# Kernel tuning notes

Hardware: AMD Instinct MI355X
Metric: run time of the kernel (lower is better)

Reference implementation:

```python
import jax, jax.numpy as jnp
import numpy as np

B, S, D, H = 2, 2048, 1024, 16
HD = D // H
NEG = -9000000000000000.0


def setup_inputs() -> dict:
    key = jax.random.key(0)
    ks = jax.random.split(key, 12)
    scale = 1.0 / np.sqrt(D)
    inp = {
        "k": jax.random.normal(ks[0], (B, S, D), jnp.float32),
        "q": jax.random.normal(ks[1], (B, S, D), jnp.float32),
        "v": jax.random.normal(ks[2], (B, S, D), jnp.float32),
        # causal mask, float (0/1), shape [B, 1, S, S] as expected by __call__
        "mask": jnp.broadcast_to(jnp.tril(jnp.ones((S, S), jnp.float32))[None, None], (B, 1, S, S)),
        "Wq": jax.random.normal(ks[3], (D, D), jnp.float32) * scale,
        "bq": jnp.zeros((D,), jnp.float32),
        "Wk": jax.random.normal(ks[4], (D, D), jnp.float32) * scale,
        "bk": jnp.zeros((D,), jnp.float32),
        "Wv": jax.random.normal(ks[5], (D, D), jnp.float32) * scale,
        "bv": jnp.zeros((D,), jnp.float32),
        "Wo": jax.random.normal(ks[6], (D, D), jnp.float32) * scale,
        "bo": jnp.zeros((D,), jnp.float32),
    }
    return inp


def _split_heads(x):
    # [B, S, D] -> [B, H, S, HD]
    return x.reshape(B, S, H, HD).transpose(0, 2, 1, 3)


def reference(k, q, v, mask, Wq, bq, Wk, bk, Wv, bv, Wo, bo):
    keys = _split_heads(k @ Wk + bk)
    queries = _split_heads(q @ Wq + bq)
    values = _split_heads(v @ Wv + bv)
    # scaled dot product with materialized scores (faithful to source)
    logits = jnp.einsum("bhqd,bhkd->bhqk", queries, keys) / np.sqrt(HD)
    logits = jnp.where(mask == 0, NEG, logits)
    attention = jax.nn.softmax(logits, axis=-1)
    out = jnp.einsum("bhqk,bhkd->bhqd", attention, values)
    out = out.transpose(0, 2, 1, 3).reshape(B, S, D)
    o = out @ Wo + bo
    return (o, attention)
```

## Files before the change

### kernel.cpp

```cpp
#include <hip/hip_runtime.h>
#include <stdint.h>

typedef unsigned short u16;
typedef short short8 __attribute__((ext_vector_type(8)));
typedef unsigned short ushort8 __attribute__((ext_vector_type(8)));
typedef float f32x4 __attribute__((ext_vector_type(4)));

#define S_LEN 2048
#define D_DIM 1024
#define H_NUM 16
#define HD_DIM 64
#define NEGBIG (-1e30f)

__device__ __forceinline__ float bf2f(u16 u) {
  union { uint32_t i; float f; } x; x.i = ((uint32_t)u) << 16; return x.f;
}
__device__ __forceinline__ u16 f2bf(float f) {
  union { float f; uint32_t i; } x; x.f = f;
  uint32_t u = x.i;
  uint32_t r = (u + 0x7fffu + ((u >> 16) & 1u)) >> 16;
  return (u16)r;
}
__device__ __forceinline__ f32x4 mfma16(short8 a, short8 b, f32x4 c) {
  return __builtin_amdgcn_mfma_f32_16x16x32_bf16(a, b, c, 0, 0, 0);
}
__device__ __forceinline__ bool mask_is_f32(const void* mask) {
  return *(const float*)mask == 1.0f;
}

__global__ __launch_bounds__(256) void conv_qkv(const void* __restrict__ q,
                                                const void* __restrict__ k,
                                                const void* __restrict__ v,
                                                u16* __restrict__ out,
                                                const void* __restrict__ mask) {
  bool isf32 = mask_is_f32(mask);
  int z = blockIdx.y;
  const void* src = (z == 0) ? q : (z == 1) ? k : v;
  size_t i = ((size_t)blockIdx.x * 256 + threadIdx.x) * 8;
  u16* dst = out + (size_t)z * 4194304;
  if (isf32) {
    const f32x4* p = (const f32x4*)((const float*)src + i);
    f32x4 a = p[0], b = p[1];
    ushort8 o;
#pragma unroll
    for (int j = 0; j < 4; j++) { o[j] = f2bf(a[j]); o[4 + j] = f2bf(b[j]); }
    *(ushort8*)(dst + i) = o;
  } else {
    *(ushort8*)(dst + i) = *(const ushort8*)((const u16*)src + i);
  }
}

__global__ __launch_bounds__(256) void wtrans(const void* __restrict__ w0,
                                              const void* __restrict__ w1,
                                              const void* __restrict__ w2,
                                              const void* __restrict__ w3,
                                              u16* __restrict__ dstBase,
                                              const void* __restrict__ mask) {
  bool isf32 = mask_is_f32(mask);
  int y = blockIdx.y;
  const void* W = (y == 0) ? w0 : (y == 1) ? w1 : (y == 2) ? w2 : w3;
  u16* out = dstBase + (size_t)y * 1048576;
  __shared__ u16 t[64][65];
  int tile = blockIdx.x;
  int r0 = (tile >> 4) * 64, c0 = (tile & 15) * 64;
  int tid = threadIdx.x;
  int rr = tid >> 6, cc = tid & 63;
#pragma unroll
  for (int i = 0; i < 16; i++) {
    int r = i * 4 + rr;
    size_t idx = (size_t)(r0 + r) * 1024 + c0 + cc;
    t[r][cc] = isf32 ? f2bf(((const float*)W)[idx]) : ((const u16*)W)[idx];
  }
  __syncthreads();
#pragma unroll
  for (int i = 0; i < 16; i++) {
    int r = i * 4 + rr;
    out[(size_t)(c0 + r) * 1024 + r0 + cc] = t[cc][r];
  }
}

__global__ __launch_bounds__(256) void conv_bias(const void* __restrict__ b0,
                                                 const void* __restrict__ b1,
                                                 const void* __restrict__ b2,
                                                 const void* __restrict__ b3,
                                                 float* __restrict__ out,
                                                 const void* __restrict__ mask) {
  bool isf32 = mask_is_f32(mask);
  int y = blockIdx.y;
  const void* b = (y == 0) ? b0 : (y == 1) ? b1 : (y == 2) ? b2 : b3;
  int i = blockIdx.x * 256 + threadIdx.x;
  float v = isf32 ? ((const float*)b)[i] : bf2f(((const u16*)b)[i]);
  out[y * 1024 + i] = v;
}

__global__ __launch_bounds__(256) void v_transpose(const u16* __restrict__ V,
                                                   u16* __restrict__ Vt) {
  __shared__ u16 t[64][65];
  int bh = blockIdx.x, st = blockIdx.y;
  int b = bh >> 4, h = bh & 15;
  int tid = threadIdx.x;
  int rr = tid >> 6, cc = tid & 63;
#pragma unroll
  for (int i = 0; i < 16; i++) {
    int r = i * 4 + rr;
    t[r][cc] = V[(size_t)(b * S_LEN + st * 64 + r) * D_DIM + h * HD_DIM + cc];
  }
  __syncthreads();
#pragma unroll
  for (int i = 0; i < 16; i++) {
    int r = i * 4 + rr;
    Vt[(size_t)(bh * HD_DIM + r) * S_LEN + st * 64 + cc] = t[cc][r];
  }
}

__device__ __forceinline__ void gemm_body(const u16* __restrict__ A,
                                          const u16* __restrict__ Bt,
                                          const float* __restrict__ bias,
                                          void* __restrict__ C, bool cf32,
                                          int M, int N, int K, int m0, int n0) {
  __shared__ __align__(16) u16 lA[2][128 * 32];
  __shared__ __align__(16) u16 lB[2][128 * 32];
  int tid = threadIdx.x;
  int lane = tid & 63, w = tid >> 6;
  int wr = w >> 1, wc = w & 1;
  f32x4 acc[4][4] = {};
  int rs = tid >> 2, c8 = tid & 3;
  ushort8 ra[2], rb[2];
  const int nk = K >> 5;
#pragma unroll
  for (int p = 0; p < 2; p++) {
    ra[p] = *(const ushort8*)(A + (size_t)(m0 + p * 64 + rs) * K + c8 * 8);
    rb[p] = *(const ushort8*)(Bt + (size_t)(n0 + p * 64 + rs) * K + c8 * 8);
  }
#pragma unroll
  for (int p = 0; p < 2; p++) {
    *(ushort8*)(&lA[0][(p * 64 + rs) * 32 + c8 * 8]) = ra[p];
    *(ushort8*)(&lB[0][(p * 64 + rs) * 32 + c8 * 8]) = rb[p];
  }
  int cur = 0;
  for (int kt = 0; kt < nk; kt++) {
    __syncthreads();
    if (kt + 1 < nk) {
#pragma unroll
      for (int p = 0; p < 2; p++) {
        ra[p] = *(const ushort8*)(A + (size_t)(m0 + p * 64 + rs) * K + (kt + 1) * 32 + c8 * 8);
        rb[p] = *(const ushort8*)(Bt + (size_t)(n0 + p * 64 + rs) * K + (kt + 1) * 32 + c8 * 8);
      }
    }
    short8 af[4], bf[4];
#pragma unroll
    for (int i = 0; i < 4; i++) {
      af[i] = *(const short8*)(&lA[cur][(wr * 64 + i * 16 + (lane & 15)) * 32 + (lane >> 4) * 8]);
      bf[i] = *(const short8*)(&lB[cur][(wc * 64 + i * 16 + (lane & 15)) * 32 + (lane >> 4) * 8]);
    }
#pragma unroll
    for (int i = 0; i < 4; i++)
#pragma unroll
      for (int j = 0; j < 4; j++)
        acc[i][j] = mfma16(af[i], bf[j], acc[i][j]);
    if (kt + 1 < nk) {
#pragma unroll
      for (int p = 0; p < 2; p++) {
        *(ushort8*)(&lA[cur ^ 1][(p * 64 + rs) * 32 + c8 * 8]) = ra[p];
        *(ushort8*)(&lB[cur ^ 1][(p * 64 + rs) * 32 + c8 * 8]) = rb[p];
      }
    }
    cur ^= 1;
  }
#pragma unroll
  for (int j = 0; j < 4; j++) {
    float bv = bias[n0 + wc * 64 + j * 16 + (lane & 15)];
#pragma unroll
    for (int i = 0; i < 4; i++) {
#pragma unroll
      for (int jj = 0; jj < 4; jj++) {
        int row = m0 + wr * 64 + i * 16 + ((lane >> 4) << 2) + jj;
        int col = n0 + wc * 64 + j * 16 + (lane & 15);
        float val = acc[i][j][jj] + bv;
        if (cf32) ((float*)C)[(size_t)row * N + col] = val;
        else ((u16*)C)[(size_t)row * N + col] = f2bf(val);
      }
    }
  }
}

__global__ __launch_bounds__(256, 2) void qkv_gemm(const u16* __restrict__ Ab,
                                                   const u16* __restrict__ WTall,
                                                   const float* __restrict__ biasF,
                                                   u16* __restrict__ outbase) {
  int z = blockIdx.z;
  gemm_body(Ab + (size_t)z * 4194304, WTall + (size_t)z * 1048576, biasF + z * 1024,
            outbase + (size_t)z * 4194304, false,
            4096, 1024, 1024, blockIdx.y * 128, blockIdx.x * 128);
}

__global__ __launch_bounds__(256, 2) void gemm_bt(const u16* __restrict__ A,
                                                  const u16* __restrict__ Bt,
                                                  const float* __restrict__ bias,
                                                  void* __restrict__ dout,
                                                  const void* __restrict__ mask) {
  bool isf32 = mask_is_f32(mask);
  gemm_body(A, Bt, bias, dout, isf32,
            4096, 1024, 1024, blockIdx.y * 128, blockIdx.x * 128);
}

__global__ __launch_bounds__(256, 3) void attn_fused(const u16* __restrict__ Qg,
                                                     const u16* __restrict__ Kg,
                                                     const u16* __restrict__ VtG,
                                                     void* __restrict__ dout,
                                                     u16* __restrict__ ctx,
                                                     const void* __restrict__ mask) {
  bool isf32 = mask_is_f32(mask);
  int x = blockIdx.x, bh = blockIdx.y;
  int b = bh >> 4, h = bh & 15;
  int tid = threadIdx.x, lane = tid & 63, w = tid >> 6;
  __shared__ __align__(16) u16 lQ[128 * 72];
  __shared__ __align__(16) u16 lK[64 * 72];
  __shared__ __align__(16) u16 lV[64 * 72];
  __shared__ __align__(16) u16 lP[64 * 72];

#pragma unroll
  for (int s = 0; s < 2; s++) {
    int qt = (s == 0) ? x : 31 - x;
    int q0 = qt * 64;
#pragma unroll
    for (int p = 0; p < 2; p++) {
      int idx = p * 256 + tid;
      int r = idx >> 3, c8i = idx & 7;
      ushort8 v = *(const ushort8*)(Qg + (size_t)(b * S_LEN + q0 + r) * D_DIM + h * HD_DIM + c8i * 8);
      *(ushort8*)(&lQ[(s * 64 + r) * 72 + c8i * 8]) = v;
    }
  }

  for (int s = 0; s < 2; s++) {
    int qt = (s == 0) ? x : 31 - x;
    int q0 = qt * 64;
    int nkv = qt + 1;

    auto stageK = [&](int kt) {
#pragma unroll
      for (int p = 0; p < 2; p++) {
        int idx = p * 256 + tid;
        int r = idx >> 3, c8i = idx & 7;
        ushort8 v = *(const ushort8*)(Kg + (size_t)(b * S_LEN + kt * 64 + r) * D_DIM + h * HD_DIM + c8i * 8);
        *(ushort8*)(&lK[r * 72 + c8i * 8]) = v;
      }
    };
    auto stageV = [&](int kt) {
#pragma unroll
      for (int p = 0; p < 2; p++) {
        int idx = p * 256 + tid;
        int r = idx >> 3, c8i = idx & 7;
        ushort8 v = *(const ushort8*)(VtG + (size_t)(bh * HD_DIM + r) * S_LEN + kt * 64 + c8i * 8);
        *(ushort8*)(&lV[r * 72 + c8i * 8]) = v;
      }
    };
    auto computeS = [&](int kt, f32x4 (&sacc)[4]) {
      short8 af[2], bfr[4][2];
#pragma unroll
      for (int ks = 0; ks < 2; ks++)
        af[ks] = *(const short8*)(&lQ[(s * 64 + w * 16 + (lane & 15)) * 72 + ks * 32 + (lane >> 4) * 8]);
#pragma unroll
      for (int j = 0; j < 4; j++)
#pragma unroll
        for (int ks = 0; ks < 2; ks++)
          bfr[j][ks] = *(const short8*)(&lK[(j * 16 + (lane & 15)) * 72 + ks * 32 + (lane >> 4) * 8]);
#pragma unroll
      for (int j = 0; j < 4; j++) {
        f32x4 a = {0.f, 0.f, 0.f, 0.f};
        a = mfma16(af[0], bfr[j][0], a);
        a = mfma16(af[1], bfr[j][1], a);
        sacc[j] = a;
      }
      bool needmask = (kt == qt);
#pragma unroll
      for (int j = 0; j < 4; j++)
#pragma unroll
        for (int jj = 0; jj < 4; jj++) {
          float sv = sacc[j][jj] * 0.125f;
          if (needmask) {
            int row = q0 + w * 16 + ((lane >> 4) << 2) + jj;
            int col = kt * 64 + j * 16 + (lane & 15);
            if (col > row) sv = NEGBIG;
          }
          sacc[j][jj] = sv;
        }
    };

    float m_[4], l_[4];
#pragma unroll
    for (int jj = 0; jj < 4; jj++) { m_[jj] = NEGBIG; l_[jj] = 0.f; }

    for (int kt = 0; kt < nkv; kt++) {
      __syncthreads();
      stageK(kt);
      __syncthreads();
      f32x4 sacc[4];
      computeS(kt, sacc);
#pragma unroll
      for (int jj = 0; jj < 4; jj++) {
        float vm = fmaxf(fmaxf(sacc[0][jj], sacc[1][jj]),
                         fmaxf(sacc[2][jj], sacc[3][jj]));
        vm = fmaxf(vm, __shfl_xor(vm, 1));
        vm = fmaxf(vm, __shfl_xor(vm, 2));
        vm = fmaxf(vm, __shfl_xor(vm, 4));
        vm = fmaxf(vm, __shfl_xor(vm, 8));
        float nm = fmaxf(m_[jj], vm);
        float ss = __expf(sacc[0][jj] - nm) + __expf(sacc[1][jj] - nm) +
                   __expf(sacc[2][jj] - nm) + __expf(sacc[3][jj] - nm);
        ss += __shfl_xor(ss, 1);
        ss += __shfl_xor(ss, 2);
        ss += __shfl_xor(ss, 4);
        ss += __shfl_xor(ss, 8);
        l_[jj] = l_[jj] * __expf(m_[jj] - nm) + ss;
        m_[jj] = nm;
      }
    }
    float invl[4];
#pragma unroll
    for (int jj = 0; jj < 4; jj++) invl[jj] = 1.f / l_[jj];

    f32x4 oacc[4] = {};

    for (int kt = 0; kt < nkv; kt++) {
      __syncthreads();
      stageK(kt);
      stageV(kt);
      __syncthreads();
      f32x4 sacc[4];
      computeS(kt, sacc);
#pragma unroll
      for (int j = 0; j < 4; j++)
#pragma unroll
        for (int jj = 0; jj < 4; jj++) {
          float p = __expf(sacc[j][jj] - m_[jj]) * invl[jj];
          lP[(w * 16 + ((lane >> 4) << 2) + jj) * 72 + j * 16 + (lane & 15)] = f2bf(p);
        }
      __syncthreads();
      {
        int rbase = tid >> 5, c2 = tid & 31;
        if (isf32) {
          float* attnF = (float*)dout + 4194304;
#pragma unroll
          for (int it = 0; it < 8; it++) {
            int r = it * 8 + rbase;
            float2 vv;
            vv.x = bf2f(lP[r * 72 + c2 * 2]);
            vv.y = bf2f(lP[r * 72 + c2 * 2 + 1]);
            *(float2*)(attnF + ((size_t)bh * S_LEN + q0 + r) * S_LEN + kt * 64 + c2 * 2) = vv;
          }
        } else {
          u16* attnB = (u16*)dout + 4194304;
#pragma unroll
          for (int it = 0; it < 8; it++) {
            int r = it * 8 + rbase;
            uint32_t vv = *(const uint32_t*)(&lP[r * 72 + c2 * 2]);
            *(uint32_t*)(attnB + ((size_t)bh * S_LEN + q0 + r) * S_LEN + kt * 64 + c2 * 2) = vv;
          }
        }
      }
      short8 pa[2], vb[4][2];
#pragma unroll
      for (int ks = 0; ks < 2; ks++)
        pa[ks] = *(const short8*)(&lP[(w * 16 + (lane & 15)) * 72 + ks * 32 + (lane >> 4) * 8]);
#pragma unroll
      for (int f = 0; f < 4; f++)
#pragma unroll
        for (int ks = 0; ks < 2; ks++)
          vb[f][ks] = *(const short8*)(&lV[(f * 16 + (lane & 15)) * 72 + ks * 32 + (lane >> 4) * 8]);
#pragma unroll
      for (int f = 0; f < 4; f++) {
        oacc[f] = mfma16(pa[0], vb[f][0], oacc[f]);
        oacc[f] = mfma16(pa[1], vb[f][1], oacc[f]);
      }
    }

    {
      int z0 = nkv * 64;
      if (isf32) {
        int zc4 = (S_LEN - z0) >> 2;
        if (zc4 > 0) {
          f32x4 zz = {0.f, 0.f, 0.f, 0.f};
          float* attnF = (float*)dout + 4194304;
          for (int r = tid >> 5; r < 64; r += 8)
            for (int c = tid & 31; c < zc4; c += 32)
              *(f32x4*)(attnF + ((size_t)bh * S_LEN + q0 + r) * S_LEN + z0 + c * 4) = zz;
        }
      } else {
        int zc8 = (S_LEN - z0) >> 3;
        if (zc8 > 0) {
          ushort8 zz = {0, 0, 0, 0, 0, 0, 0, 0};
          u16* attnB = (u16*)dout + 4194304;
          for (int r = tid >> 5; r < 64; r += 8)
            for (int c = tid & 31; c < zc8; c += 32)
              *(ushort8*)(attnB + ((size_t)bh * S_LEN + q0 + r) * S_LEN + z0 + c * 8) = zz;
        }
      }
    }

#pragma unroll
    for (int f = 0; f < 4; f++)
#pragma unroll
      for (int jj = 0; jj < 4; jj++) {
        int row = q0 + w * 16 + ((lane >> 4) << 2) + jj;
        int col = h * HD_DIM + f * 16 + (lane & 15);
        ctx[(size_t)(b * S_LEN + row) * D_DIM + col] = f2bf(oacc[f][jj]);
      }
  }
}

extern "C" void kernel_launch(void* const* d_in, const int* in_sizes, int n_in,
                              void* d_out, int out_size, void* d_ws, size_t ws_size,
                              hipStream_t stream) {
  const void* kin = d_in[0];
  const void* qin = d_in[1];
  const void* vin = d_in[2];
  const void* mask = d_in[3];
  const void* Wq = d_in[4];
  const void* bq = d_in[5];
  const void* Wk = d_in[6];
  const void* bk = d_in[7];
  const void* Wv = d_in[8];
  const void* bv = d_in[9];
  const void* Wo = d_in[10];
  const void* bo = d_in[11];

  u16* ws = (u16*)d_ws;
  u16* WT = ws;
  float* biasF = (float*)(ws + 4 * 1048576);
  u16* Cb = ws + 4 * 1048576 + 8192;
  u16* Qp = Cb + 3 * 4194304;
  u16* Kp = Qp + 4194304;
  u16* Vp = Kp + 4194304;
  u16* Vt = Vp + 4194304;
  u16* ctx = Vt + 4194304;

  conv_qkv<<<dim3(2048, 3), 256, 0, stream>>>(qin, kin, vin, Cb, mask);
  wtrans<<<dim3(256, 4), 256, 0, stream>>>(Wq, Wk, Wv, Wo, WT, mask);
  conv_bias<<<dim3(4, 4), 256, 0, stream>>>(bq, bk, bv, bo, biasF, mask);
  qkv_gemm<<<dim3(8, 32, 3), 256, 0, stream>>>(Cb, WT, biasF, Qp);
  v_transpose<<<dim3(32, 32), 256, 0, stream>>>(Vp, Vt);
  attn_fused<<<dim3(16, 32), 256, 0, stream>>>(Qp, Kp, Vt, d_out, ctx, mask);
  gemm_bt<<<dim3(8, 32), 256, 0, stream>>>(ctx, WT + 3 * 1048576, biasF + 3072, d_out, mask);
}
```

Baseline: 294.6 us.

## Double-buffer K/V tiles in attention and use async global-to-LDS loads in GEMM

The GEMM now stages A/B tiles straight into LDS with global_load_lds, prefetching the next k-tile while the MFMAs run, with one barrier per iteration. The attention kernel double-buffers K and V in LDS with register prefetch, keeps Q fragments in registers instead of LDS, and writes the attention probabilities directly from registers rather than through an LDS round-trip. This removes barriers and lets loads overlap with compute. In exchange, the direct attention-matrix stores are scalar and less coalesced, and the attention kernel's occupancy hint drops from 3 to 2 blocks per CU.

```diff
diff --git a/kernel.cpp b/kernel.cpp
--- a/kernel.cpp
+++ b/kernel.cpp
@@ -26,6 +26,11 @@
 }
 __device__ __forceinline__ bool mask_is_f32(const void* mask) {
   return *(const float*)mask == 1.0f;
+}
+__device__ __forceinline__ void async_cp16(const u16* g, u16* l) {
+  __builtin_amdgcn_global_load_lds((const __attribute__((address_space(1))) unsigned int*)g,
+                                   (__attribute__((address_space(3))) unsigned int*)l,
+                                   16, 0, 0);
 }
 
 __global__ __launch_bounds__(256) void conv_qkv(const void* __restrict__ q,
@@ -124,29 +129,24 @@
   int lane = tid & 63, w = tid >> 6;
   int wr = w >> 1, wc = w & 1;
   f32x4 acc[4][4] = {};
-  int rs = tid >> 2, c8 = tid & 3;
-  ushort8 ra[2], rb[2];
   const int nk = K >> 5;
-#pragma unroll
-  for (int p = 0; p < 2; p++) {
-    ra[p] = *(const ushort8*)(A + (size_t)(m0 + p * 64 + rs) * K + c8 * 8);
-    rb[p] = *(const ushort8*)(Bt + (size_t)(n0 + p * 64 + rs) * K + c8 * 8);
-  }
-#pragma unroll
-  for (int p = 0; p < 2; p++) {
-    *(ushort8*)(&lA[0][(p * 64 + rs) * 32 + c8 * 8]) = ra[p];
-    *(ushort8*)(&lB[0][(p * 64 + rs) * 32 + c8 * 8]) = rb[p];
-  }
+  int grow = lane >> 2, gcol = (lane & 3) * 8;
+
+#define GEMM_ISSUE(kt, buf)                                                              \
+  {                                                                                      \
+    _Pragma("unroll") for (int p = 0; p < 2; p++) {                                      \
+      async_cp16(A + (size_t)(m0 + p * 64 + w * 16 + grow) * K + (kt) * 32 + gcol,       \
+                 &lA[buf][p * 2048 + w * 512]);                                          \
+      async_cp16(Bt + (size_t)(n0 + p * 64 + w * 16 + grow) * K + (kt) * 32 + gcol,      \
+                 &lB[buf][p * 2048 + w * 512]);                                          \
+    }                                                                                    \
+  }
+
+  GEMM_ISSUE(0, 0);
+  __syncthreads();
   int cur = 0;
   for (int kt = 0; kt < nk; kt++) {
-    __syncthreads();
-    if (kt + 1 < nk) {
-#pragma unroll
-      for (int p = 0; p < 2; p++) {
-        ra[p] = *(const ushort8*)(A + (size_t)(m0 + p * 64 + rs) * K + (kt + 1) * 32 + c8 * 8);
-        rb[p] = *(const ushort8*)(Bt + (size_t)(n0 + p * 64 + rs) * K + (kt + 1) * 32 + c8 * 8);
-      }
-    }
+    if (kt + 1 < nk) GEMM_ISSUE(kt + 1, cur ^ 1);
     short8 af[4], bf[4];
 #pragma unroll
     for (int i = 0; i < 4; i++) {
@@ -158,15 +158,10 @@
 #pragma unroll
       for (int j = 0; j < 4; j++)
         acc[i][j] = mfma16(af[i], bf[j], acc[i][j]);
-    if (kt + 1 < nk) {
-#pragma unroll
-      for (int p = 0; p < 2; p++) {
-        *(ushort8*)(&lA[cur ^ 1][(p * 64 + rs) * 32 + c8 * 8]) = ra[p];
-        *(ushort8*)(&lB[cur ^ 1][(p * 64 + rs) * 32 + c8 * 8]) = rb[p];
-      }
-    }
+    __syncthreads();
     cur ^= 1;
   }
+#undef GEMM_ISSUE
 #pragma unroll
   for (int j = 0; j < 4; j++) {
     float bv = bias[n0 + wc * 64 + j * 16 + (lane & 15)];
@@ -204,7 +199,7 @@
             4096, 1024, 1024, blockIdx.y * 128, blockIdx.x * 128);
 }
 
-__global__ __launch_bounds__(256, 3) void attn_fused(const u16* __restrict__ Qg,
+__global__ __launch_bounds__(256, 2) void attn_fused(const u16* __restrict__ Qg,
                                                      const u16* __restrict__ Kg,
                                                      const u16* __restrict__ VtG,
                                                      void* __restrict__ dout,
@@ -214,62 +209,60 @@
   int x = blockIdx.x, bh = blockIdx.y;
   int b = bh >> 4, h = bh & 15;
   int tid = threadIdx.x, lane = tid & 63, w = tid >> 6;
-  __shared__ __align__(16) u16 lQ[128 * 72];
-  __shared__ __align__(16) u16 lK[64 * 72];
-  __shared__ __align__(16) u16 lV[64 * 72];
+  __shared__ __align__(16) u16 lK[2][64 * 72];
+  __shared__ __align__(16) u16 lV[2][64 * 72];
   __shared__ __align__(16) u16 lP[64 * 72];
 
-#pragma unroll
-  for (int s = 0; s < 2; s++) {
-    int qt = (s == 0) ? x : 31 - x;
-    int q0 = qt * 64;
-#pragma unroll
-    for (int p = 0; p < 2; p++) {
-      int idx = p * 256 + tid;
-      int r = idx >> 3, c8i = idx & 7;
-      ushort8 v = *(const ushort8*)(Qg + (size_t)(b * S_LEN + q0 + r) * D_DIM + h * HD_DIM + c8i * 8);
-      *(ushort8*)(&lQ[(s * 64 + r) * 72 + c8i * 8]) = v;
-    }
-  }
+  float* attnF = (float*)dout + 4194304;
+  u16* attnB = (u16*)dout + 4194304;
+  int sr = tid >> 3, sc8 = (tid & 7) * 8;
 
   for (int s = 0; s < 2; s++) {
     int qt = (s == 0) ? x : 31 - x;
     int q0 = qt * 64;
     int nkv = qt + 1;
 
-    auto stageK = [&](int kt) {
-#pragma unroll
-      for (int p = 0; p < 2; p++) {
-        int idx = p * 256 + tid;
-        int r = idx >> 3, c8i = idx & 7;
-        ushort8 v = *(const ushort8*)(Kg + (size_t)(b * S_LEN + kt * 64 + r) * D_DIM + h * HD_DIM + c8i * 8);
-        *(ushort8*)(&lK[r * 72 + c8i * 8]) = v;
-      }
+    short8 qf[2];
+#pragma unroll
+    for (int ks = 0; ks < 2; ks++)
+      qf[ks] = *(const short8*)(Qg + (size_t)(b * S_LEN + q0 + w * 16 + (lane & 15)) * D_DIM +
+                                h * HD_DIM + ks * 32 + (lane >> 4) * 8);
+
+    ushort8 kreg[2], vreg[2];
+    auto loadK = [&](int kt) {
+#pragma unroll
+      for (int p = 0; p < 2; p++)
+        kreg[p] = *(const ushort8*)(Kg + (size_t)(b * S_LEN + kt * 64 + p * 32 + sr) * D_DIM +
+                                    h * HD_DIM + sc8);
     };
-    auto stageV = [&](int kt) {
-#pragma unroll
-      for (int p = 0; p < 2; p++) {
-        int idx = p * 256 + tid;
-        int r = idx >> 3, c8i = idx & 7;
-        ushort8 v = *(const ushort8*)(VtG + (size_t)(bh * HD_DIM + r) * S_LEN + kt * 64 + c8i * 8);
-        *(ushort8*)(&lV[r * 72 + c8i * 8]) = v;
-      }
+    auto writeK = [&](int buf) {
+#pragma unroll
+      for (int p = 0; p < 2; p++)
+        *(ushort8*)(&lK[buf][(p * 32 + sr) * 72 + sc8]) = kreg[p];
     };
-    auto computeS = [&](int kt, f32x4 (&sacc)[4]) {
-      short8 af[2], bfr[4][2];
-#pragma unroll
-      for (int ks = 0; ks < 2; ks++)
-        af[ks] = *(const short8*)(&lQ[(s * 64 + w * 16 + (lane & 15)) * 72 + ks * 32 + (lane >> 4) * 8]);
+    auto loadV = [&](int kt) {
+#pragma unroll
+      for (int p = 0; p < 2; p++)
+        vreg[p] = *(const ushort8*)(VtG + (size_t)(bh * HD_DIM + p * 32 + sr) * S_LEN +
+                                    kt * 64 + sc8);
+    };
+    auto writeV = [&](int buf) {
+#pragma unroll
+      for (int p = 0; p < 2; p++)
+        *(ushort8*)(&lV[buf][(p * 32 + sr) * 72 + sc8]) = vreg[p];
+    };
+    auto computeS = [&](int buf, int kt, f32x4 (&sacc)[4]) {
+      short8 bfr[4][2];
 #pragma unroll
       for (int j = 0; j < 4; j++)
 #pragma unroll
         for (int ks = 0; ks < 2; ks++)
-          bfr[j][ks] = *(const short8*)(&lK[(j * 16 + (lane & 15)) * 72 + ks * 32 + (lane >> 4) * 8]);
+          bfr[j][ks] = *(const short8*)(&lK[buf][(j * 16 + (lane & 15)) * 72 + ks * 32 + (lane >> 4) * 8]);
 #pragma unroll
       for (int j = 0; j < 4; j++) {
         f32x4 a = {0.f, 0.f, 0.f, 0.f};
-        a = mfma16(af[0], bfr[j][0], a);
-        a = mfma16(af[1], bfr[j][1], a);
+        a = mfma16(qf[0], bfr[j][0], a);
+        a = mfma16(qf[1], bfr[j][1], a);
         sacc[j] = a;
       }
       bool needmask = (kt == qt);
@@ -291,12 +284,13 @@
 #pragma unroll
     for (int jj = 0; jj < 4; jj++) { m_[jj] = NEGBIG; l_[jj] = 0.f; }
 
+    loadK(0); writeK(0);
+    __syncthreads();
+    int cur = 0;
     for (int kt = 0; kt < nkv; kt++) {
-      __syncthreads();
-      stageK(kt);
-      __syncthreads();
+      if (kt + 1 < nkv) loadK(kt + 1);
       f32x4 sacc[4];
-      computeS(kt, sacc);
+      computeS(cur, kt, sacc);
 #pragma unroll
       for (int jj = 0; jj < 4; jj++) {
         float vm = fmaxf(fmaxf(sacc[0][jj], sacc[1][jj]),
@@ -315,6 +309,9 @@
         l_[jj] = l_[jj] * __expf(m_[jj] - nm) + ss;
         m_[jj] = nm;
       }
+      if (kt + 1 < nkv) writeK(cur ^ 1);
+      __syncthreads();
+      cur ^= 1;
     }
     float invl[4];
 #pragma unroll
@@ -322,43 +319,24 @@
 
     f32x4 oacc[4] = {};
 
+    loadK(0); loadV(0); writeK(0); writeV(0);
+    __syncthreads();
+    cur = 0;
     for (int kt = 0; kt < nkv; kt++) {
-      __syncthreads();
-      stageK(kt);
-      stageV(kt);
-      __syncthreads();
+      if (kt + 1 < nkv) { loadK(kt + 1); loadV(kt + 1); }
       f32x4 sacc[4];
-      computeS(kt, sacc);
+      computeS(cur, kt, sacc);
 #pragma unroll
       for (int j = 0; j < 4; j++)
 #pragma unroll
         for (int jj = 0; jj < 4; jj++) {
           float p = __expf(sacc[j][jj] - m_[jj]) * invl[jj];
+          int row = q0 + w * 16 + ((lane >> 4) << 2) + jj;
+          int col = kt * 64 + j * 16 + (lane & 15);
+          if (isf32) attnF[((size_t)bh * S_LEN + row) * S_LEN + col] = p;
+          else attnB[((size_t)bh * S_LEN + row) * S_LEN + col] = f2bf(p);
           lP[(w * 16 + ((lane >> 4) << 2) + jj) * 72 + j * 16 + (lane & 15)] = f2bf(p);
         }
-      __syncthreads();
-      {
-        int rbase = tid >> 5, c2 = tid & 31;
-        if (isf32) {
-          float* attnF = (float*)dout + 4194304;
-#pragma unroll
-          for (int it = 0; it < 8; it++) {
-            int r = it * 8 + rbase;
-            float2 vv;
-            vv.x = bf2f(lP[r * 72 + c2 * 2]);
-            vv.y = bf2f(lP[r * 72 + c2 * 2 + 1]);
-            *(float2*)(attnF + ((size_t)bh * S_LEN + q0 + r) * S_LEN + kt * 64 + c2 * 2) = vv;
-          }
-        } else {
-          u16* attnB = (u16*)dout + 4194304;
-#pragma unroll
-          for (int it = 0; it < 8; it++) {
-            int r = it * 8 + rbase;
-            uint32_t vv = *(const uint32_t*)(&lP[r * 72 + c2 * 2]);
-            *(uint32_t*)(attnB + ((size_t)bh * S_LEN + q0 + r) * S_LEN + kt * 64 + c2 * 2) = vv;
-          }
-        }
-      }
       short8 pa[2], vb[4][2];
 #pragma unroll
       for (int ks = 0; ks < 2; ks++)
@@ -367,12 +345,15 @@
       for (int f = 0; f < 4; f++)
 #pragma unroll
         for (int ks = 0; ks < 2; ks++)
-          vb[f][ks] = *(const short8*)(&lV[(f * 16 + (lane & 15)) * 72 + ks * 32 + (lane >> 4) * 8]);
+          vb[f][ks] = *(const short8*)(&lV[cur][(f * 16 + (lane & 15)) * 72 + ks * 32 + (lane >> 4) * 8]);
 #pragma unroll
       for (int f = 0; f < 4; f++) {
         oacc[f] = mfma16(pa[0], vb[f][0], oacc[f]);
         oacc[f] = mfma16(pa[1], vb[f][1], oacc[f]);
       }
+      if (kt + 1 < nkv) { writeK(cur ^ 1); writeV(cur ^ 1); }
+      __syncthreads();
+      cur ^= 1;
     }
 
     {
@@ -381,7 +362,6 @@
         int zc4 = (S_LEN - z0) >> 2;
         if (zc4 > 0) {
           f32x4 zz = {0.f, 0.f, 0.f, 0.f};
-          float* attnF = (float*)dout + 4194304;
           for (int r = tid >> 5; r < 64; r += 8)
             for (int c = tid & 31; c < zc4; c += 32)
               *(f32x4*)(attnF + ((size_t)bh * S_LEN + q0 + r) * S_LEN + z0 + c * 4) = zz;
@@ -390,7 +370,6 @@
         int zc8 = (S_LEN - z0) >> 3;
         if (zc8 > 0) {
           ushort8 zz = {0, 0, 0, 0, 0, 0, 0, 0};
-          u16* attnB = (u16*)dout + 4194304;
           for (int r = tid >> 5; r < 64; r += 8)
             for (int c = tid & 31; c < zc8; c += 32)
               *(ushort8*)(attnB + ((size_t)bh * S_LEN + q0 + r) * S_LEN + z0 + c * 8) = zz;
```

New measurement: 299.1 us. About the same (+1.5%).
